# Optimization experiments

Hardware: AMD Instinct MI355X
Metric: run time of the kernel (lower is better)

The kernel has to match this reference:

```python
import jax, jax.numpy as jnp
import numpy as np

N_NODES = 50000
N_EDGES = 800000
IN_CH = 64
HID_CH = 64
OUT_CH = 2


def setup_inputs() -> dict:
    key = jax.random.key(0)
    ks = jax.random.split(key, 7)
    x = jax.random.normal(ks[0], (N_NODES, IN_CH), dtype=jnp.float32)
    edge_index = jax.random.randint(ks[1], (2, N_EDGES), 0, N_NODES, dtype=jnp.int64)
    # Glorot-ish scaled weights (PyG SAGEConv uses glorot init)
    W1_l = jax.random.normal(ks[2], (HID_CH, IN_CH), dtype=jnp.float32) * (1.0 / np.sqrt(IN_CH))
    W1_r = jax.random.normal(ks[3], (HID_CH, IN_CH), dtype=jnp.float32) * (1.0 / np.sqrt(IN_CH))
    b1 = jnp.zeros((HID_CH,), dtype=jnp.float32)
    W2_l = jax.random.normal(ks[4], (OUT_CH, HID_CH), dtype=jnp.float32) * (1.0 / np.sqrt(HID_CH))
    W2_r = jax.random.normal(ks[5], (OUT_CH, HID_CH), dtype=jnp.float32) * (1.0 / np.sqrt(HID_CH))
    b2 = jnp.zeros((OUT_CH,), dtype=jnp.float32)
    return {"x": x, "edge_index": edge_index, "W1_l": W1_l, "W1_r": W1_r,
            "b1": b1, "W2_l": W2_l, "W2_r": W2_r, "b2": b2}


def _sage_conv(h, src, dst, n_nodes, Wl, Wr, b):
    # mean-aggregate neighbor messages h[src] at dst
    msg = h[src]                                                  # [E, d] gather
    agg = jax.ops.segment_sum(msg, dst, num_segments=n_nodes)    # [N, d]
    deg = jax.ops.segment_sum(jnp.ones((src.shape[0],), h.dtype), dst,
                              num_segments=n_nodes)              # [N]
    mean = agg / jnp.maximum(deg, 1.0)[:, None]
    # PyG SAGEConv: lin_l(aggr) + lin_r(x_root); lin_l has bias
    return mean @ Wl.T + b + h @ Wr.T


def reference(x, edge_index, W1_l, W1_r, b1, W2_l, W2_r, b2):
    src, dst = edge_index[0], edge_index[1]
    n = x.shape[0]
    h = jax.nn.relu(_sage_conv(x, src, dst, n, W1_l, W1_r, b1))
    # dropout(p=0.5) is identity in eval mode
    out = _sage_conv(h, src, dst, n, W2_l, W2_r, b2)
    return out
```

## Files before the change

kernel.cpp:

```cpp
#include <hip/hip_runtime.h>
#include <hip/hip_bf16.h>

static constexpr int NN = 50000;
static constexpr int NE = 800000;
static constexpr int CH = 64;

static constexpr int BKN    = 256;
static constexpr int NBKT   = (NN + BKN - 1) / BKN;
static constexpr int CHUNK  = 4096;
static constexpr int NBIN   = (NE + CHUNK - 1) / CHUNK;
static constexpr int SUBCAP = 64;
static constexpr int COLCAP = 4608;
static constexpr int NCVT   = (NN * CH / 8 + 255) / 256;

__global__ __launch_bounds__(256) void k_prep(
        const float* __restrict__ x, __hip_bfloat16* __restrict__ xb,
        const float* __restrict__ W1l, const float* __restrict__ W1r,
        float* __restrict__ WlT, float* __restrict__ WrT,
        const int* __restrict__ src, const int* __restrict__ dst,
        int* __restrict__ lcnt, unsigned int* __restrict__ bstage) {
    const int tid = threadIdx.x;
    if (blockIdx.x < NCVT) {
        const int base = (blockIdx.x * 256 + tid) * 8;
        if (base < NN * CH) {
            float4 v0 = *(const float4*)(x + base);
            float4 v1 = *(const float4*)(x + base + 4);
            union { unsigned short us[8]; uint4 u4; } o;
            __hip_bfloat16 h;
            h = __float2bfloat16(v0.x); o.us[0] = *(unsigned short*)&h;
            h = __float2bfloat16(v0.y); o.us[1] = *(unsigned short*)&h;
            h = __float2bfloat16(v0.z); o.us[2] = *(unsigned short*)&h;
            h = __float2bfloat16(v0.w); o.us[3] = *(unsigned short*)&h;
            h = __float2bfloat16(v1.x); o.us[4] = *(unsigned short*)&h;
            h = __float2bfloat16(v1.y); o.us[5] = *(unsigned short*)&h;
            h = __float2bfloat16(v1.z); o.us[6] = *(unsigned short*)&h;
            h = __float2bfloat16(v1.w); o.us[7] = *(unsigned short*)&h;
            *(uint4*)(xb + base) = o.u4;
        }
        if (blockIdx.x == 0) {
            for (int i = tid; i < CH * CH; i += 256) {
                int c = i >> 6, o = i & 63;
                WlT[i] = W1l[o * CH + c];
                WrT[i] = W1r[o * CH + c];
            }
        }
    } else {
        const int blk = blockIdx.x - NCVT;
        __shared__ int cnt[NBKT];
        if (tid < NBKT) cnt[tid] = 0;
        __syncthreads();
        const int e0 = blk * CHUNK;
#pragma unroll
        for (int i = 0; i < 16; ++i) {
            int e = e0 + i * 256 + tid;
            if (e < NE) {
                int d = dst[e];
                int b = d >> 8;
                int r = atomicAdd(&cnt[b], 1);
                if (r < SUBCAP)
                    bstage[((size_t)b * NBIN + blk) * SUBCAP + r] =
                        (unsigned)src[e] | ((unsigned)(d & (BKN - 1)) << 16);
            }
        }
        __syncthreads();
        if (tid < NBKT) lcnt[blk * NBKT + tid] = min(cnt[tid], SUBCAP);
    }
}

__global__ __launch_bounds__(256) void k_sort(
        const unsigned int* __restrict__ bstage, const int* __restrict__ lcnt,
        int* __restrict__ begv, int* __restrict__ degv, int* __restrict__ col) {
    __shared__ int ccnt[256];
    __shared__ int ncnt[BKN];
    __shared__ int wsum[4];
    const int b   = blockIdx.x;
    const int tid = threadIdx.x;
    const int lane = tid & 63, w = tid >> 6;

    ccnt[tid] = (tid < NBIN) ? lcnt[tid * NBKT + b] : 0;
    ncnt[tid] = 0;
    __syncthreads();

    if (tid < NBIN) {
        const unsigned int* cp = bstage + ((size_t)b * NBIN + tid) * SUBCAP;
        const int c = ccnt[tid];
        int j = 0;
        for (; j + 4 <= c; j += 4) {
            unsigned w0 = cp[j], w1 = cp[j + 1], w2 = cp[j + 2], w3 = cp[j + 3];
            atomicAdd(&ncnt[w0 >> 16], 1);
            atomicAdd(&ncnt[w1 >> 16], 1);
            atomicAdd(&ncnt[w2 >> 16], 1);
            atomicAdd(&ncnt[w3 >> 16], 1);
        }
        for (; j < c; ++j) atomicAdd(&ncnt[cp[j] >> 16], 1);
    }
    __syncthreads();

    const int v = ncnt[tid];
    int s = v;
#pragma unroll
    for (int off = 1; off < 64; off <<= 1) {
        int t = __shfl_up(s, off);
        if (lane >= off) s += t;
    }
    if (lane == 63) wsum[w] = s;
    __syncthreads();
    if (tid == 0) {
        int c = 0;
#pragma unroll
        for (int k = 0; k < 4; ++k) { int t = wsum[k]; wsum[k] = c; c += t; }
    }
    __syncthreads();
    const int excl = wsum[w] + s - v;
    const int n = b * BKN + tid;
    if (n < NN) { begv[n] = b * COLCAP + excl; degv[n] = v; }
    __syncthreads();
    ncnt[tid] = excl;
    __syncthreads();

    if (tid < NBIN) {
        const unsigned int* cp = bstage + ((size_t)b * NBIN + tid) * SUBCAP;
        const int c = ccnt[tid];
        int* cb = col + (size_t)b * COLCAP;
        for (int j = 0; j < c; ++j) {
            unsigned wd = cp[j];
            int r = atomicAdd(&ncnt[wd >> 16], 1);
            cb[r] = (int)(wd & 0xFFFFu);
        }
    }
}

__global__ __launch_bounds__(256) void k_agg1(const int* __restrict__ begv,
                                              const int* __restrict__ degv,
                                              const int* __restrict__ col,
                                              const unsigned short* __restrict__ xbu,
                                              float* __restrict__ mean) {
    const int node = blockIdx.x * 4 + (threadIdx.x >> 6);
    const int lane = threadIdx.x & 63;
    const int g = lane >> 4;
    const int s = lane & 15;
    if (node >= NN) return;
    const int beg = begv[node], dg = degv[node];
    const int end = beg + dg;
    float a0 = 0.f, a1 = 0.f, a2 = 0.f, a3 = 0.f;
    int i = beg;
    for (; i + 8 <= end; i += 8) {
        const int eA = col[i + g];
        const int eB = col[i + 4 + g];
        ushort4 ua = *(const ushort4*)(xbu + eA * CH + s * 4);
        ushort4 ub = *(const ushort4*)(xbu + eB * CH + s * 4);
        a0 += __uint_as_float((unsigned)ua.x << 16) + __uint_as_float((unsigned)ub.x << 16);
        a1 += __uint_as_float((unsigned)ua.y << 16) + __uint_as_float((unsigned)ub.y << 16);
        a2 += __uint_as_float((unsigned)ua.z << 16) + __uint_as_float((unsigned)ub.z << 16);
        a3 += __uint_as_float((unsigned)ua.w << 16) + __uint_as_float((unsigned)ub.w << 16);
    }
    for (; i < end; i += 4) {
        if (g < end - i) {
            const int e = col[i + g];
            ushort4 u = *(const ushort4*)(xbu + e * CH + s * 4);
            a0 += __uint_as_float((unsigned)u.x << 16);
            a1 += __uint_as_float((unsigned)u.y << 16);
            a2 += __uint_as_float((unsigned)u.z << 16);
            a3 += __uint_as_float((unsigned)u.w << 16);
        }
    }
    a0 += __shfl_xor(a0, 16); a0 += __shfl_xor(a0, 32);
    a1 += __shfl_xor(a1, 16); a1 += __shfl_xor(a1, 32);
    a2 += __shfl_xor(a2, 16); a2 += __shfl_xor(a2, 32);
    a3 += __shfl_xor(a3, 16); a3 += __shfl_xor(a3, 32);
    if (lane < 16) {
        const float inv = dg ? 1.0f / (float)dg : 0.0f;
        *(float4*)(mean + (size_t)node * CH + lane * 4) =
            make_float4(a0 * inv, a1 * inv, a2 * inv, a3 * inv);
    }
}

__global__ __launch_bounds__(256, 2) void k_fused(
        const float* __restrict__ x, const float* __restrict__ mean,
        const float* __restrict__ WlT, const float* __restrict__ WrT,
        const float* __restrict__ b1,
        const float* __restrict__ W2l, const float* __restrict__ W2r,
        const float* __restrict__ b2,
        float* __restrict__ hl2, float* __restrict__ out) {
    __shared__ float As[32][132];
    __shared__ float Ws[128][64];
    const int tid = threadIdx.x;
    const int n0 = blockIdx.x * 32;

    for (int idx = tid; idx < 1024; idx += 256) {
        int part = idx >> 9, rem = idx & 511, row = rem >> 4, q = rem & 15;
        int n = n0 + row;
        float4 v = make_float4(0.f, 0.f, 0.f, 0.f);
        if (n < NN) {
            const float* sp = part ? (x + (size_t)n * CH) : (mean + (size_t)n * CH);
            v = *(const float4*)(sp + q * 4);
        }
        *(float4*)&As[row][part * 64 + q * 4] = v;
    }
    for (int idx = tid; idx < 2048; idx += 256) {
        int r = idx >> 4, q = idx & 15;
        const float* wp = (r < 64) ? (WlT + r * CH) : (WrT + (r - 64) * CH);
        *(float4*)&Ws[r][q * 4] = *(const float4*)(wp + q * 4);
    }
    __syncthreads();

    const int nd0 = (tid >> 4) * 2;
    const int oc0 = (tid & 15) * 4;
    float acc[2][4] = {{0.f, 0.f, 0.f, 0.f}, {0.f, 0.f, 0.f, 0.f}};

    for (int kb = 0; kb < 32; ++kb) {
        float4 a0 = *(const float4*)&As[nd0][kb * 4];
        float4 a1 = *(const float4*)&As[nd0 + 1][kb * 4];
        float4 w0 = *(const float4*)&Ws[kb * 4 + 0][oc0];
        float4 w1 = *(const float4*)&Ws[kb * 4 + 1][oc0];
        float4 w2 = *(const float4*)&Ws[kb * 4 + 2][oc0];
        float4 w3 = *(const float4*)&Ws[kb * 4 + 3][oc0];
#pragma unroll
        for (int j = 0; j < 4; ++j) {
            const float u0 = ((const float*)&w0)[j];
            const float u1 = ((const float*)&w1)[j];
            const float u2 = ((const float*)&w2)[j];
            const float u3 = ((const float*)&w3)[j];
            acc[0][j] = fmaf(a0.x, u0, fmaf(a0.y, u1, fmaf(a0.z, u2, fmaf(a0.w, u3, acc[0][j]))));
            acc[1][j] = fmaf(a1.x, u0, fmaf(a1.y, u1, fmaf(a1.z, u2, fmaf(a1.w, u3, acc[1][j]))));
        }
    }

    float b1v[4], wl0[4], wl1[4], wr0[4], wr1[4];
#pragma unroll
    for (int j = 0; j < 4; ++j) {
        b1v[j] = b1[oc0 + j];
        wl0[j] = W2l[oc0 + j];  wl1[j] = W2l[64 + oc0 + j];
        wr0[j] = W2r[oc0 + j];  wr1[j] = W2r[64 + oc0 + j];
    }
    const float b20 = b2[0], b21 = b2[1];
#pragma unroll
    for (int nd = 0; nd < 2; ++nd) {
        float a0 = 0.f, a1 = 0.f, r0 = 0.f, r1 = 0.f;
#pragma unroll
        for (int j = 0; j < 4; ++j) {
            const float h = fmaxf(acc[nd][j] + b1v[j], 0.0f);
            a0 = fmaf(h, wl0[j], a0);
            a1 = fmaf(h, wl1[j], a1);
            r0 = fmaf(h, wr0[j], r0);
            r1 = fmaf(h, wr1[j], r1);
        }
#pragma unroll
        for (int off = 1; off < 16; off <<= 1) {
            a0 += __shfl_xor(a0, off);
            a1 += __shfl_xor(a1, off);
            r0 += __shfl_xor(r0, off);
            r1 += __shfl_xor(r1, off);
        }
        const int n = n0 + nd0 + nd;
        if ((tid & 15) == 0 && n < NN) {
            *(float2*)(hl2 + (size_t)n * 2) = make_float2(a0, a1);
            *(float2*)(out + (size_t)n * 2) = make_float2(b20 + r0, b21 + r1);
        }
    }
}

__global__ __launch_bounds__(256) void k_agg2(const int* __restrict__ begv,
                                              const int* __restrict__ degv,
                                              const int* __restrict__ col,
                                              const float2* __restrict__ hl2,
                                              float2* __restrict__ out) {
    int t = blockIdx.x * 256 + threadIdx.x;
    int node = t >> 3;
    int sl = t & 7;
    if (node >= NN) return;
    const int beg = begv[node], dg = degv[node];
    const int end = beg + dg;
    float ax = 0.0f, ay = 0.0f;
    for (int i = beg + sl; i < end; i += 8) {
        float2 v = hl2[col[i]];
        ax += v.x; ay += v.y;
    }
#pragma unroll
    for (int off = 4; off > 0; off >>= 1) {
        ax += __shfl_xor(ax, off);
        ay += __shfl_xor(ay, off);
    }
    if (sl == 0) {
        const float inv = dg ? 1.0f / (float)dg : 0.0f;
        float2 o = out[node];
        o.x += ax * inv;
        o.y += ay * inv;
        out[node] = o;
    }
}

extern "C" void kernel_launch(void* const* d_in, const int* in_sizes, int n_in,
                              void* d_out, int out_size, void* d_ws, size_t ws_size,
                              hipStream_t stream) {
    const float* x   = (const float*)d_in[0];
    const int*   ei  = (const int*)d_in[1];
    const float* W1l = (const float*)d_in[2];
    const float* W1r = (const float*)d_in[3];
    const float* b1  = (const float*)d_in[4];
    const float* W2l = (const float*)d_in[5];
    const float* W2r = (const float*)d_in[6];
    const float* b2  = (const float*)d_in[7];
    float* out = (float*)d_out;

    const int* src = ei;
    const int* dst = ei + NE;

    char* wsp = (char*)d_ws;
    int*          lcnt   = (int*)wsp;
    int*          begv   = lcnt + NBIN * NBKT;
    int*          degv   = begv + 50048;
    unsigned int* bstage = (unsigned int*)(degv + 50048);
    int*          col    = (int*)(bstage + (size_t)NBKT * NBIN * SUBCAP);
    float*        mean   = (float*)(col + (size_t)NBKT * COLCAP);
    float*        hl2    = mean + (size_t)NN * CH;
    __hip_bfloat16* xbf  = (__hip_bfloat16*)(hl2 + (size_t)NN * 2);
    float*        WlT    = (float*)(xbf + (size_t)NN * CH);
    float*        WrT    = WlT + CH * CH;

    k_prep<<<NCVT + NBIN, 256, 0, stream>>>(x, xbf, W1l, W1r, WlT, WrT,
                                            src, dst, lcnt, bstage);
    k_sort<<<NBKT, 256, 0, stream>>>(bstage, lcnt, begv, degv, col);
    k_agg1<<<(NN + 3) / 4, 256, 0, stream>>>(begv, degv, col,
                                             (const unsigned short*)xbf, mean);
    k_fused<<<(NN + 31) / 32, 256, 0, stream>>>(
        x, mean, WlT, WrT, b1, W2l, W2r, b2, hl2, out);
    k_agg2<<<(8 * NN + 255) / 256, 256, 0, stream>>>(
        begv, degv, col, (const float2*)hl2, (float2*)out);
}
```

Baseline: 82.64 us.

## Fuse layer-1 neighbor aggregation into the dense transform kernel

Layer-1 mean aggregation now runs inside the dense transform kernel: each wave aggregates 8 rows of bf16 neighbor features and writes the means straight into shared memory, in place of a separate kernel that wrote a float32 mean buffer to global memory. This removes one launch and a full N×64 float write and read-back. The cost is fewer waves in flight for the latency-bound gather, since there are 1563 blocks at 2 per CU with 8 serial rows per wave, compared with 4 waves each owning one node before.

```diff
diff --git a/kernel.cpp b/kernel.cpp
--- a/kernel.cpp
+++ b/kernel.cpp
@@ -130,53 +130,10 @@
     }
 }
 
-__global__ __launch_bounds__(256) void k_agg1(const int* __restrict__ begv,
-                                              const int* __restrict__ degv,
-                                              const int* __restrict__ col,
-                                              const unsigned short* __restrict__ xbu,
-                                              float* __restrict__ mean) {
-    const int node = blockIdx.x * 4 + (threadIdx.x >> 6);
-    const int lane = threadIdx.x & 63;
-    const int g = lane >> 4;
-    const int s = lane & 15;
-    if (node >= NN) return;
-    const int beg = begv[node], dg = degv[node];
-    const int end = beg + dg;
-    float a0 = 0.f, a1 = 0.f, a2 = 0.f, a3 = 0.f;
-    int i = beg;
-    for (; i + 8 <= end; i += 8) {
-        const int eA = col[i + g];
-        const int eB = col[i + 4 + g];
-        ushort4 ua = *(const ushort4*)(xbu + eA * CH + s * 4);
-        ushort4 ub = *(const ushort4*)(xbu + eB * CH + s * 4);
-        a0 += __uint_as_float((unsigned)ua.x << 16) + __uint_as_float((unsigned)ub.x << 16);
-        a1 += __uint_as_float((unsigned)ua.y << 16) + __uint_as_float((unsigned)ub.y << 16);
-        a2 += __uint_as_float((unsigned)ua.z << 16) + __uint_as_float((unsigned)ub.z << 16);
-        a3 += __uint_as_float((unsigned)ua.w << 16) + __uint_as_float((unsigned)ub.w << 16);
-    }
-    for (; i < end; i += 4) {
-        if (g < end - i) {
-            const int e = col[i + g];
-            ushort4 u = *(const ushort4*)(xbu + e * CH + s * 4);
-            a0 += __uint_as_float((unsigned)u.x << 16);
-            a1 += __uint_as_float((unsigned)u.y << 16);
-            a2 += __uint_as_float((unsigned)u.z << 16);
-            a3 += __uint_as_float((unsigned)u.w << 16);
-        }
-    }
-    a0 += __shfl_xor(a0, 16); a0 += __shfl_xor(a0, 32);
-    a1 += __shfl_xor(a1, 16); a1 += __shfl_xor(a1, 32);
-    a2 += __shfl_xor(a2, 16); a2 += __shfl_xor(a2, 32);
-    a3 += __shfl_xor(a3, 16); a3 += __shfl_xor(a3, 32);
-    if (lane < 16) {
-        const float inv = dg ? 1.0f / (float)dg : 0.0f;
-        *(float4*)(mean + (size_t)node * CH + lane * 4) =
-            make_float4(a0 * inv, a1 * inv, a2 * inv, a3 * inv);
-    }
-}
-
-__global__ __launch_bounds__(256, 2) void k_fused(
-        const float* __restrict__ x, const float* __restrict__ mean,
+__global__ __launch_bounds__(256, 2) void k_aggfu(
+        const float* __restrict__ x,
+        const int* __restrict__ begv, const int* __restrict__ degv,
+        const int* __restrict__ col, const unsigned short* __restrict__ xbu,
         const float* __restrict__ WlT, const float* __restrict__ WrT,
         const float* __restrict__ b1,
         const float* __restrict__ W2l, const float* __restrict__ W2r,
@@ -187,20 +144,66 @@
     const int tid = threadIdx.x;
     const int n0 = blockIdx.x * 32;
 
-    for (int idx = tid; idx < 1024; idx += 256) {
-        int part = idx >> 9, rem = idx & 511, row = rem >> 4, q = rem & 15;
+    for (int idx = tid; idx < 512; idx += 256) {
+        int row = idx >> 4, q = idx & 15;
         int n = n0 + row;
         float4 v = make_float4(0.f, 0.f, 0.f, 0.f);
-        if (n < NN) {
-            const float* sp = part ? (x + (size_t)n * CH) : (mean + (size_t)n * CH);
-            v = *(const float4*)(sp + q * 4);
-        }
-        *(float4*)&As[row][part * 64 + q * 4] = v;
+        if (n < NN) v = *(const float4*)(x + (size_t)n * CH + q * 4);
+        *(float4*)&As[row][64 + q * 4] = v;
     }
     for (int idx = tid; idx < 2048; idx += 256) {
         int r = idx >> 4, q = idx & 15;
         const float* wp = (r < 64) ? (WlT + r * CH) : (WrT + (r - 64) * CH);
         *(float4*)&Ws[r][q * 4] = *(const float4*)(wp + q * 4);
+    }
+
+    {
+        const int w    = tid >> 6;
+        const int lane = tid & 63;
+        const int g = lane >> 4;
+        const int s = lane & 15;
+#pragma unroll
+        for (int rr = 0; rr < 8; ++rr) {
+            const int row = w * 8 + rr;
+            const int n = n0 + row;
+            float a0 = 0.f, a1 = 0.f, a2 = 0.f, a3 = 0.f;
+            int dg = 0;
+            if (n < NN) {
+                const int beg = begv[n];
+                dg = degv[n];
+                const int end = beg + dg;
+                int i = beg;
+                for (; i + 8 <= end; i += 8) {
+                    const int eA = col[i + g];
+                    const int eB = col[i + 4 + g];
+                    ushort4 ua = *(const ushort4*)(xbu + eA * CH + s * 4);
+                    ushort4 ub = *(const ushort4*)(xbu + eB * CH + s * 4);
+                    a0 += __uint_as_float((unsigned)ua.x << 16) + __uint_as_float((unsigned)ub.x << 16);
+                    a1 += __uint_as_float((unsigned)ua.y << 16) + __uint_as_float((unsigned)ub.y << 16);
+                    a2 += __uint_as_float((unsigned)ua.z << 16) + __uint_as_float((unsigned)ub.z << 16);
+                    a3 += __uint_as_float((unsigned)ua.w << 16) + __uint_as_float((unsigned)ub.w << 16);
+                }
+                for (; i < end; i += 4) {
+                    if (g < end - i) {
+                        const int e = col[i + g];
+                        ushort4 u = *(const ushort4*)(xbu + e * CH + s * 4);
+                        a0 += __uint_as_float((unsigned)u.x << 16);
+                        a1 += __uint_as_float((unsigned)u.y << 16);
+                        a2 += __uint_as_float((unsigned)u.z << 16);
+                        a3 += __uint_as_float((unsigned)u.w << 16);
+                    }
+                }
+            }
+            a0 += __shfl_xor(a0, 16); a0 += __shfl_xor(a0, 32);
+            a1 += __shfl_xor(a1, 16); a1 += __shfl_xor(a1, 32);
+            a2 += __shfl_xor(a2, 16); a2 += __shfl_xor(a2, 32);
+            a3 += __shfl_xor(a3, 16); a3 += __shfl_xor(a3, 32);
+            if (lane < 16) {
+                const float inv = dg ? 1.0f / (float)dg : 0.0f;
+                *(float4*)&As[row][lane * 4] =
+                    make_float4(a0 * inv, a1 * inv, a2 * inv, a3 * inv);
+            }
+        }
     }
     __syncthreads();
 
@@ -312,8 +315,7 @@
     int*          degv   = begv + 50048;
     unsigned int* bstage = (unsigned int*)(degv + 50048);
     int*          col    = (int*)(bstage + (size_t)NBKT * NBIN * SUBCAP);
-    float*        mean   = (float*)(col + (size_t)NBKT * COLCAP);
-    float*        hl2    = mean + (size_t)NN * CH;
+    float*        hl2    = (float*)(col + (size_t)NBKT * COLCAP);
     __hip_bfloat16* xbf  = (__hip_bfloat16*)(hl2 + (size_t)NN * 2);
     float*        WlT    = (float*)(xbf + (size_t)NN * CH);
     float*        WrT    = WlT + CH * CH;
@@ -321,10 +323,9 @@
     k_prep<<<NCVT + NBIN, 256, 0, stream>>>(x, xbf, W1l, W1r, WlT, WrT,
                                             src, dst, lcnt, bstage);
     k_sort<<<NBKT, 256, 0, stream>>>(bstage, lcnt, begv, degv, col);
-    k_agg1<<<(NN + 3) / 4, 256, 0, stream>>>(begv, degv, col,
-                                             (const unsigned short*)xbf, mean);
-    k_fused<<<(NN + 31) / 32, 256, 0, stream>>>(
-        x, mean, WlT, WrT, b1, W2l, W2r, b2, hl2, out);
+    k_aggfu<<<(NN + 31) / 32, 256, 0, stream>>>(
+        x, begv, degv, col, (const unsigned short*)xbf,
+        WlT, WrT, b1, W2l, W2r, b2, hl2, out);
     k_agg2<<<(8 * NN + 255) / 256, 256, 0, stream>>>(
         begv, degv, col, (const float2*)hl2, (float2*)out);
 }
```

New measurement: 110.1 us. 33.2% more time.
